# Performance work log

Hardware: AMD Instinct MI355X
Metric: run time of the kernel (lower is better)

The kernel has to match this reference:

```python
import jax, jax.numpy as jnp
import numpy as np

B, LA, LS, C, H = 4, 1536, 512, 256, 4
DK = C // H
NEG = -jnp.inf


def _pad(lengths, maxlen):
    # True where padded (idx >= length)
    return jnp.arange(maxlen)[None, :] >= lengths[:, None]


def build_mask(l_v, l_s, ilens, ylens):
    """Additive float mask [B, l_v+l_s, l_v+l_s] with 0 / -inf, matching
    generate_multi_modal_mask_new."""
    b = ilens.shape[0]
    i = jnp.arange(l_s)
    causal = jnp.where(i[:, None] >= i[None, :], 0.0, NEG)            # [l_s, l_s]
    tgt_pad = _pad(ylens, l_s)                                        # [b, l_s]
    mask_s_s = jnp.where(tgt_pad[:, None, :], NEG, causal[None])      # [b, l_s, l_s]
    src_row = jnp.where(_pad(ilens, l_v), NEG, 0.0)                   # [b, l_v]
    mask_v_v = jnp.broadcast_to(src_row[:, None, :], (b, l_v, l_v))
    mask_s_v = jnp.broadcast_to(src_row[:, None, :], (b, l_s, l_v))
    mask_v_s = jnp.full((b, l_v, l_s), NEG, dtype=jnp.float32)
    top = jnp.concatenate([mask_v_v, mask_v_s], axis=2)
    bot = jnp.concatenate([mask_s_v, mask_s_s], axis=2)
    return jnp.concatenate([top, bot], axis=1)


def setup_inputs() -> dict:
    key = jax.random.key(0)
    ks = jax.random.split(key, 12)
    scale = 1.0 / np.sqrt(C)
    return {
        "audio_encoder_out": jax.random.normal(ks[0], (B, LA, C), jnp.float32),
        "text_encoder_out": jax.random.normal(ks[1], (B, LS, C), jnp.float32),
        "speech_length": jax.random.randint(ks[2], (B,), 1, LA),
        "text_length": jax.random.randint(ks[3], (B,), 1, LS),
        "Wq": jax.random.normal(ks[4], (C, C), jnp.float32) * scale,
        "bq": jax.random.normal(ks[5], (C,), jnp.float32) * scale,
        "Wk": jax.random.normal(ks[6], (C, C), jnp.float32) * scale,
        "bk": jax.random.normal(ks[7], (C,), jnp.float32) * scale,
        "Wv": jax.random.normal(ks[8], (C, C), jnp.float32) * scale,
        "bv": jax.random.normal(ks[9], (C,), jnp.float32) * scale,
        "Wo": jax.random.normal(ks[10], (C, C), jnp.float32) * scale,
        "bo": jax.random.normal(ks[11], (C,), jnp.float32) * scale,
    }


def reference(audio_encoder_out, text_encoder_out, speech_length, text_length,
              Wq, bq, Wk, bk, Wv, bv, Wo, bo):
    b, l_a, c = audio_encoder_out.shape
    l_s = text_encoder_out.shape[1]
    x = jnp.concatenate([audio_encoder_out, text_encoder_out], axis=1)  # [B, L, C]
    L = l_a + l_s

    def heads(W, bias):
        return (x @ W.T + bias).reshape(b, L, H, DK).transpose(0, 2, 1, 3)  # [B,H,L,DK]

    q, k, v = heads(Wq, bq), heads(Wk, bk), heads(Wv, bv)
    scores = jnp.einsum("bhqd,bhkd->bhqk", q, k) / np.float32(np.sqrt(DK))

    amask = build_mask(l_a, l_s, speech_length, text_length)  # additive [B,L,L]
    # Faithful to torch: mask.eq(0) positions (additive-0) are filled with -inf,
    # then zeroed in attn (the module's inverted masking behavior).
    eq0 = (amask == 0.0)[:, None, :, :]                       # [B,1,L,L]
    scores = jnp.where(eq0, NEG, scores)
    attn = jax.nn.softmax(scores, axis=-1)
    attn = jnp.where(eq0, 0.0, attn)                          # (dropout = identity, eval)
    out = jnp.einsum("bhqk,bhkd->bhqd", attn, v)
    out = out.transpose(0, 2, 1, 3).reshape(b, L, H * DK)
    return out @ Wo.T + bo
```

## Files before the change

kernel.cpp:

```cpp
#include <hip/hip_runtime.h>
#include <hip/hip_bf16.h>
#include <math.h>

#define LA 1536
#define LS 512
#define LT 2048
#define CC 256
#define NH 4
#define DKH 64
#define NB 4
#define NT (LT / 64)
#define NTA (LA / 64)
#define SZ ((size_t)NB * LT * CC)

#define QSCALE 0.1803368801111244f

typedef _Float16 f16;
typedef __attribute__((ext_vector_type(8))) _Float16 f16x8;
typedef __attribute__((ext_vector_type(4))) _Float16 f16x4;
typedef __attribute__((ext_vector_type(4))) float f32x4;

__device__ inline f16x8 cvt8(const float4 a, const float4 b) {
    f16x8 h;
    h[0] = (_Float16)a.x; h[1] = (_Float16)a.y; h[2] = (_Float16)a.z; h[3] = (_Float16)a.w;
    h[4] = (_Float16)b.x; h[5] = (_Float16)b.y; h[6] = (_Float16)b.z; h[7] = (_Float16)b.w;
    return h;
}

#define PROW(j) (((j) & 32) | ((((j) >> 2) & 1) << 4) | ((((j) >> 3) & 3) << 2) | ((j) & 3))

__global__ __launch_bounds__(256) void qkv_mfma(
    const float* __restrict__ audio, const float* __restrict__ text,
    const float* __restrict__ Wq, const float* __restrict__ bq,
    const float* __restrict__ Wk, const float* __restrict__ bk,
    const float* __restrict__ Wv, const float* __restrict__ bv,
    f16* __restrict__ Qh, f16* __restrict__ Kh, f16* __restrict__ Vth)
{
    __shared__ f16 smem[128 * 64 + 64 * 64];
    f16* As = smem;
    f16* Bs = smem + 128 * 64;

    const int tid = threadIdx.x;
    const int w = tid >> 6, l = tid & 63;
    const int g = l >> 4, r = l & 15;

    const int m0 = blockIdx.x * 128;
    const int n0 = blockIdx.y * 64;
    const int mat = n0 >> 8;
    const int ch0 = n0 & 255;

    const float* W    = (mat == 0) ? Wq : (mat == 1) ? Wk : Wv;
    const float* bias = (mat == 0) ? bq : (mat == 1) ? bk : bv;

    const int b  = m0 >> 11;
    const int l0 = m0 & 2047;

    f32x4 acc[2][4] = {};

    for (int k0 = 0; k0 < CC; k0 += 64) {
        #pragma unroll
        for (int m = 0; m < 4; ++m) {
            const int idx = m * 256 + tid;
            const int row = idx >> 3, c = idx & 7;
            const int lrow = l0 + row;
            const float* src = (lrow < LA)
                ? (audio + ((size_t)b * LA + lrow) * CC + k0 + c * 8)
                : (text  + ((size_t)b * LS + (lrow - LA)) * CC + k0 + c * 8);
            const float4 x0 = *(const float4*)src;
            const float4 x1 = *(const float4*)(src + 4);
            *(f16x8*)(As + row * 64 + ((c ^ (row & 7)) << 3)) = cvt8(x0, x1);
        }
        #pragma unroll
        for (int m = 0; m < 2; ++m) {
            const int idx = m * 256 + tid;
            const int row = idx >> 3, c = idx & 7;
            const float* src = W + (size_t)(ch0 + row) * CC + k0 + c * 8;
            const float4 x0 = *(const float4*)src;
            const float4 x1 = *(const float4*)(src + 4);
            *(f16x8*)(Bs + row * 64 + ((c ^ (row & 7)) << 3)) = cvt8(x0, x1);
        }
        __syncthreads();
        #pragma unroll
        for (int kc = 0; kc < 2; ++kc) {
            f16x8 af[2];
            #pragma unroll
            for (int i = 0; i < 2; ++i) {
                const int row = w * 32 + i * 16 + r;
                const int c = kc * 4 + g;
                af[i] = *(const f16x8*)(As + row * 64 + ((c ^ (row & 7)) << 3));
            }
            f16x8 bf[4];
            #pragma unroll
            for (int j = 0; j < 4; ++j) {
                const int row = j * 16 + r;
                const int c = kc * 4 + g;
                bf[j] = *(const f16x8*)(Bs + row * 64 + ((c ^ (row & 7)) << 3));
            }
            #pragma unroll
            for (int i = 0; i < 2; ++i)
                #pragma unroll
                for (int j = 0; j < 4; ++j)
                    acc[i][j] = __builtin_amdgcn_mfma_f32_16x16x32_f16(af[i], bf[j], acc[i][j], 0, 0, 0);
        }
        __syncthreads();
    }

    float bcol[4];
    #pragma unroll
    for (int j = 0; j < 4; ++j) bcol[j] = bias[ch0 + j * 16 + r];

    if (mat <= 1) {
        f16* Out = (mat == 0) ? Qh : Kh;
        const float osc = (mat == 0) ? QSCALE : 1.0f;
        #pragma unroll
        for (int i = 0; i < 2; ++i)
            #pragma unroll
            for (int e = 0; e < 4; ++e) {
                const int m = m0 + w * 32 + i * 16 + g * 4 + e;
                #pragma unroll
                for (int j = 0; j < 4; ++j)
                    Out[(size_t)m * CC + ch0 + j * 16 + r] =
                        (_Float16)((acc[i][j][e] + bcol[j]) * osc);
            }
    } else {
        f16* Ts = smem;
        #pragma unroll
        for (int i = 0; i < 2; ++i)
            #pragma unroll
            for (int e = 0; e < 4; ++e) {
                const int ml = w * 32 + i * 16 + g * 4 + e;
                #pragma unroll
                for (int j = 0; j < 4; ++j)
                    Ts[(j * 16 + r) * 136 + ml] = (_Float16)(acc[i][j][e] + bcol[j]);
            }
        __syncthreads();
        const int b2 = m0 >> 11, l0m = m0 & 2047;
        #pragma unroll
        for (int u = 0; u < 4; ++u) {
            const int idx = u * 256 + tid;
            const int nl = idx >> 4, mc = idx & 15;
            const f16x8 vv = *(const f16x8*)(Ts + nl * 136 + mc * 8);
            const int nglob = ch0 + nl;
            const int hh = nglob >> 6, dd = nglob & 63;
            *(f16x8*)(Vth + ((size_t)((b2 * NH + hh) * DKH + dd)) * LT + l0m + mc * 8) = vv;
        }
    }
}

__global__ __launch_bounds__(512) void attn_f16(
    const f16* __restrict__ Q, const f16* __restrict__ K,
    const f16* __restrict__ Vt,
    const int* __restrict__ slen, const int* __restrict__ tlen,
    f16* __restrict__ AO)
{
    __shared__ __align__(16) f16 KsA[2][2 * 4096];
    __shared__ __align__(16) f16 VtsA[2][2 * 4096];

    const int tid = threadIdx.x;
    const int w = tid >> 6, l = tid & 63;
    const int gid = w >> 2, wg = w & 3;
    const int g = l >> 4, r = l & 15;
    const int tg = tid & 255;

    const int q0 = blockIdx.x * 64;
    const int h  = blockIdx.y;
    const int b  = blockIdx.z;

    const int ilen = slen[b];
    const int kcap = LA + tlen[b];
    const int nskip = ilen >> 6;
    int ntskip = 0;
    if (q0 >= LA) {
        const int skipmax = min(q0 - 63, kcap - 64);
        const int d = skipmax - LA;
        ntskip = (d < 0) ? 0 : ((d >> 6) + 1);
    }
    const int nAudio = NTA - nskip;
    const int nProc  = nAudio + (NT - NTA) - ntskip;
    const int nIter  = (nProc + 1) >> 1;

    const int qrow = q0 + 16 * wg + r;

    f16x8 qf[2];
    #pragma unroll
    for (int ch = 0; ch < 2; ++ch)
        qf[ch] = *(const f16x8*)(Q + ((size_t)(b * LT) + qrow) * CC + h * DKH + ch * 32 + g * 8);

    const int srow0 = tg >> 3, scc = tg & 7;
    const int srow1 = srow0 + 32;
    const int kp0 = PROW(srow0), kp1 = PROW(srow1);
    const int kdst0 = kp0 * 64 + ((scc ^ (kp0 & 7)) << 3);
    const int kdst1 = kp1 * 64 + ((scc ^ (kp1 & 7)) << 3);
    const int vdst0 = srow0 * 64 + ((scc ^ (srow0 & 7)) << 3);
    const int vdst1 = srow1 * 64 + ((scc ^ (srow1 & 7)) << 3);

    #define TILE_OF(p) ((p) < nAudio ? (nskip + (p)) : (NTA + ntskip + ((p) - nAudio)))

    {
        const int k0 = TILE_OF(gid) * 64;
        *(f16x8*)(KsA[gid] + kdst0) =
            *(const f16x8*)(K + ((size_t)(b * LT) + k0 + srow0) * CC + h * DKH + scc * 8);
        *(f16x8*)(KsA[gid] + kdst1) =
            *(const f16x8*)(K + ((size_t)(b * LT) + k0 + srow1) * CC + h * DKH + scc * 8);
        *(f16x8*)(VtsA[gid] + vdst0) =
            *(const f16x8*)(Vt + ((size_t)((b * NH + h) * DKH) + srow0) * LT + k0 + scc * 8);
        *(f16x8*)(VtsA[gid] + vdst1) =
            *(const f16x8*)(Vt + ((size_t)((b * NH + h) * DKH) + srow1) * LT + k0 + scc * 8);
    }
    __syncthreads();

    float m_run = -1e30f, l_run = 0.0f;
    f32x4 o[4] = {};

    int cur = 0;
    for (int i = 0; i < nIter; ++i) {
        const int pcur = 2 * i + gid;
        const bool curV = pcur < nProc;
        const bool nxtV = (pcur + 2) < nProc;

        f16x8 kr0, kr1, vr0, vr1;
        if (nxtV) {
            const int kn = TILE_OF(pcur + 2) * 64;
            kr0 = *(const f16x8*)(K + ((size_t)(b * LT) + kn + srow0) * CC + h * DKH + scc * 8);
            kr1 = *(const f16x8*)(K + ((size_t)(b * LT) + kn + srow1) * CC + h * DKH + scc * 8);
            vr0 = *(const f16x8*)(Vt + ((size_t)((b * NH + h) * DKH) + srow0) * LT + kn + scc * 8);
            vr1 = *(const f16x8*)(Vt + ((size_t)((b * NH + h) * DKH) + srow1) * LT + kn + scc * 8);
        }

        if (curV) {
            const int kt = TILE_OF(pcur);
            const int k0 = kt * 64;
            const f16* Kb = KsA[gid] + cur * 4096;
            const f16* Vb = VtsA[gid] + cur * 4096;

            f32x4 sacc[4] = {};
            #pragma unroll
            for (int s = 0; s < 4; ++s) {
                const int arow = 16 * s + r;
                #pragma unroll
                for (int ch = 0; ch < 2; ++ch) {
                    const f16x8 a = *(const f16x8*)(Kb + arow * 64 + (((ch * 4 + g) ^ (arow & 7)) << 3));
                    sacc[s] = __builtin_amdgcn_mfma_f32_16x16x32_f16(a, qf[ch], sacc[s], 0, 0, 0);
                }
            }

            const int mode = (kt < NTA) ? ((k0 >= ilen) ? 0 : 1)
                                        : ((q0 < LA) ? 0 : 2);
            const int kb = k0 + 8 * g;
            float sv[16];
            if (mode == 0) {
                #pragma unroll
                for (int s = 0; s < 4; ++s)
                    #pragma unroll
                    for (int e = 0; e < 4; ++e) sv[s * 4 + e] = sacc[s][e];
            } else if (mode == 1) {
                #pragma unroll
                for (int s = 0; s < 4; ++s)
                    #pragma unroll
                    for (int e = 0; e < 4; ++e) {
                        const int kk = kb + 32 * (s >> 1) + 4 * (s & 1) + e;
                        sv[s * 4 + e] = (kk >= ilen) ? sacc[s][e] : -INFINITY;
                    }
            } else {
                #pragma unroll
                for (int s = 0; s < 4; ++s)
                    #pragma unroll
                    for (int e = 0; e < 4; ++e) {
                        const int kk = kb + 32 * (s >> 1) + 4 * (s & 1) + e;
                        sv[s * 4 + e] = (kk > qrow || kk >= kcap) ? sacc[s][e] : -INFINITY;
                    }
            }

            float mloc = -1e30f;
            #pragma unroll
            for (int u = 0; u < 16; ++u) mloc = fmaxf(mloc, sv[u]);
            mloc = fmaxf(mloc, __shfl_xor(mloc, 16));
            mloc = fmaxf(mloc, __shfl_xor(mloc, 32));
            const float m_new = fmaxf(m_run, mloc);

            float ssum = 0.0f;
            f16x4 ph[4];
            #pragma unroll
            for (int s = 0; s < 4; ++s)
                #pragma unroll
                for (int e = 0; e < 4; ++e) {
                    const float p = exp2f(sv[s * 4 + e] - m_new);
                    ph[s][e] = (_Float16)p;
                    ssum += p;
                }
            ssum += __shfl_xor(ssum, 16);
            ssum += __shfl_xor(ssum, 32);

            if (__all(m_new == m_run)) {
                l_run += ssum;
            } else {
                const float sc = exp2f(m_run - m_new);
                l_run = l_run * sc + ssum;
                m_run = m_new;
                #pragma unroll
                for (int e = 0; e < 4; ++e) {
                    const float scr = __shfl(sc, 4 * g + e);
                    #pragma unroll
                    for (int dsb = 0; dsb < 4; ++dsb) o[dsb][e] *= scr;
                }
            }

            #pragma unroll
            for (int ch = 0; ch < 2; ++ch) {
                f16x8 a;
                #pragma unroll
                for (int e = 0; e < 4; ++e) { a[e] = ph[2 * ch][e]; a[4 + e] = ph[2 * ch + 1][e]; }
                #pragma unroll
                for (int dsb = 0; dsb < 4; ++dsb) {
                    const int vrow = 16 * dsb + r;
                    const f16x8 bf = *(const f16x8*)(Vb + vrow * 64 + (((ch * 4 + g) ^ (vrow & 7)) << 3));
                    o[dsb] = __builtin_amdgcn_mfma_f32_16x16x32_f16(a, bf, o[dsb], 0, 0, 0);
                }
            }
        }

        if (nxtV) {
            f16* Kn = KsA[gid] + (cur ^ 1) * 4096;
            f16* Vn = VtsA[gid] + (cur ^ 1) * 4096;
            *(f16x8*)(Kn + kdst0) = kr0;
            *(f16x8*)(Kn + kdst1) = kr1;
            *(f16x8*)(Vn + vdst0) = vr0;
            *(f16x8*)(Vn + vdst1) = vr1;
        }
        __syncthreads();
        cur ^= 1;
    }

    float* OcF = (float*)&KsA[0][0];
    float* ML1 = (float*)&VtsA[0][0];
    if (gid == 1) {
        #pragma unroll
        for (int dsb = 0; dsb < 4; ++dsb)
            *(f32x4*)(OcF + ((wg * 4 + dsb) << 8) + (l << 2)) = o[dsb];
        if (g == 0) {
            ML1[(16 * wg + r) * 2 + 0] = m_run;
            ML1[(16 * wg + r) * 2 + 1] = l_run;
        }
    }
    __syncthreads();

    if (gid == 0) {
        #pragma unroll
        for (int e = 0; e < 4; ++e) {
            const int qloc = 16 * wg + 4 * g + e;
            const float m0v = __shfl(m_run, 4 * g + e);
            const float l0v = __shfl(l_run, 4 * g + e);
            const float m1v = ML1[qloc * 2 + 0];
            const float l1v = ML1[qloc * 2 + 1];
            const float mt = fmaxf(m0v, m1v);
            const float c0 = exp2f(m0v - mt);
            const float c1 = exp2f(m1v - mt);
            const float inv = 1.0f / (l0v * c0 + l1v * c1);
            #pragma unroll
            for (int dsb = 0; dsb < 4; ++dsb) {
                const float v = (o[dsb][e] * c0
                               + OcF[((wg * 4 + dsb) << 8) + (l << 2) + e] * c1) * inv;
                AO[((size_t)(b * LT) + q0 + qloc) * CC + h * DKH + 16 * dsb + r] = (_Float16)v;
            }
        }
    }
    #undef TILE_OF
}

__global__ __launch_bounds__(256) void out_mfma(
    const f16* __restrict__ X, const float* __restrict__ Wo,
    const float* __restrict__ bo, float* __restrict__ Out)
{
    __shared__ f16 As[128 * 64];
    __shared__ f16 Bs[64 * 64];

    const int tid = threadIdx.x;
    const int w = tid >> 6, l = tid & 63;
    const int g = l >> 4, r = l & 15;

    const int m0 = blockIdx.x * 128;
    const int n0 = blockIdx.y * 64;

    f32x4 acc[2][4] = {};

    for (int k0 = 0; k0 < CC; k0 += 64) {
        #pragma unroll
        for (int m = 0; m < 4; ++m) {
            const int idx = m * 256 + tid;
            const int row = idx >> 3, c = idx & 7;
            *(f16x8*)(As + row * 64 + ((c ^ (row & 7)) << 3)) =
                *(const f16x8*)(X + (size_t)(m0 + row) * CC + k0 + c * 8);
        }
        #pragma unroll
        for (int m = 0; m < 2; ++m) {
            const int idx = m * 256 + tid;
            const int row = idx >> 3, c = idx & 7;
            const float* src = Wo + (size_t)(n0 + row) * CC + k0 + c * 8;
            const float4 x0 = *(const float4*)src;
            const float4 x1 = *(const float4*)(src + 4);
            *(f16x8*)(Bs + row * 64 + ((c ^ (row & 7)) << 3)) = cvt8(x0, x1);
        }
        __syncthreads();
        #pragma unroll
        for (int kc = 0; kc < 2; ++kc) {
            f16x8 af[2];
            #pragma unroll
            for (int i = 0; i < 2; ++i) {
                const int row = w * 32 + i * 16 + r;
                const int c = kc * 4 + g;
                af[i] = *(const f16x8*)(As + row * 64 + ((c ^ (row & 7)) << 3));
            }
            f16x8 bf[4];
            #pragma unroll
            for (int j = 0; j < 4; ++j) {
                const int row = j * 16 + r;
                const int c = kc * 4 + g;
                bf[j] = *(const f16x8*)(Bs + row * 64 + ((c ^ (row & 7)) << 3));
            }
            #pragma unroll
            for (int i = 0; i < 2; ++i)
                #pragma unroll
                for (int j = 0; j < 4; ++j)
                    acc[i][j] = __builtin_amdgcn_mfma_f32_16x16x32_f16(af[i], bf[j], acc[i][j], 0, 0, 0);
        }
        __syncthreads();
    }

    float bcol[4];
    #pragma unroll
    for (int j = 0; j < 4; ++j) bcol[j] = bo[n0 + j * 16 + r];

    #pragma unroll
    for (int i = 0; i < 2; ++i)
        #pragma unroll
        for (int e = 0; e < 4; ++e) {
            const int m = m0 + w * 32 + i * 16 + g * 4 + e;
            #pragma unroll
            for (int j = 0; j < 4; ++j)
                Out[(size_t)m * CC + n0 + j * 16 + r] = acc[i][j][e] + bcol[j];
        }
}

extern "C" void kernel_launch(void* const* d_in, const int* in_sizes, int n_in,
                              void* d_out, int out_size, void* d_ws, size_t ws_size,
                              hipStream_t stream)
{
    const float* audio = (const float*)d_in[0];
    const float* text  = (const float*)d_in[1];
    const int*   slen  = (const int*)d_in[2];
    const int*   tlen  = (const int*)d_in[3];
    const float* Wq = (const float*)d_in[4];
    const float* bq = (const float*)d_in[5];
    const float* Wk = (const float*)d_in[6];
    const float* bk = (const float*)d_in[7];
    const float* Wv = (const float*)d_in[8];
    const float* bv = (const float*)d_in[9];
    const float* Wo = (const float*)d_in[10];
    const float* bo = (const float*)d_in[11];
    float* out = (float*)d_out;

    f16* Qh  = (f16*)d_ws;
    f16* Kh  = Qh + SZ;
    f16* Vth = Kh + SZ;
    f16* AOh = Vth + SZ;

    qkv_mfma<<<dim3(64, 12), 256, 0, stream>>>(audio, text, Wq, bq, Wk, bk, Wv, bv,
                                               Qh, Kh, Vth);
    attn_f16<<<dim3(LT / 64, NH, NB), 512, 0, stream>>>(Qh, Kh, Vth, slen, tlen, AOh);
    out_mfma<<<dim3(64, 4), 256, 0, stream>>>(AOh, Wo, bo, out);
}
```

Measured before the change: 51.13 us.

## Fuse QKV projections per block, single-buffer attention K/V with priority hints

```diff
diff --git a/kernel.cpp b/kernel.cpp
--- a/kernel.cpp
+++ b/kernel.cpp
@@ -36,31 +36,28 @@
     const float* __restrict__ Wv, const float* __restrict__ bv,
     f16* __restrict__ Qh, f16* __restrict__ Kh, f16* __restrict__ Vth)
 {
-    __shared__ f16 smem[128 * 64 + 64 * 64];
+    __shared__ f16 smem[4 * 4096];
     f16* As = smem;
-    f16* Bs = smem + 128 * 64;
 
     const int tid = threadIdx.x;
     const int w = tid >> 6, l = tid & 63;
     const int g = l >> 4, r = l & 15;
 
-    const int m0 = blockIdx.x * 128;
-    const int n0 = blockIdx.y * 64;
-    const int mat = n0 >> 8;
-    const int ch0 = n0 & 255;
-
-    const float* W    = (mat == 0) ? Wq : (mat == 1) ? Wk : Wv;
-    const float* bias = (mat == 0) ? bq : (mat == 1) ? bk : bv;
+    const int m0  = blockIdx.x * 64;
+    const int ch0 = blockIdx.y * 64;
+
+    const float* Ws[3]   = {Wq, Wk, Wv};
+    const float* Bias[3] = {bq, bk, bv};
 
     const int b  = m0 >> 11;
     const int l0 = m0 & 2047;
 
-    f32x4 acc[2][4] = {};
+    f32x4 acc[3][4] = {};
 
     for (int k0 = 0; k0 < CC; k0 += 64) {
         #pragma unroll
-        for (int m = 0; m < 4; ++m) {
-            const int idx = m * 256 + tid;
+        for (int u = 0; u < 2; ++u) {
+            const int idx = u * 256 + tid;
             const int row = idx >> 3, c = idx & 7;
             const int lrow = l0 + row;
             const float* src = (lrow < LA)
@@ -71,79 +68,70 @@
             *(f16x8*)(As + row * 64 + ((c ^ (row & 7)) << 3)) = cvt8(x0, x1);
         }
         #pragma unroll
-        for (int m = 0; m < 2; ++m) {
-            const int idx = m * 256 + tid;
-            const int row = idx >> 3, c = idx & 7;
-            const float* src = W + (size_t)(ch0 + row) * CC + k0 + c * 8;
-            const float4 x0 = *(const float4*)src;
-            const float4 x1 = *(const float4*)(src + 4);
-            *(f16x8*)(Bs + row * 64 + ((c ^ (row & 7)) << 3)) = cvt8(x0, x1);
-        }
+        for (int mat = 0; mat < 3; ++mat)
+            #pragma unroll
+            for (int u = 0; u < 2; ++u) {
+                const int idx = u * 256 + tid;
+                const int row = idx >> 3, c = idx & 7;
+                const float* src = Ws[mat] + (size_t)(ch0 + row) * CC + k0 + c * 8;
+                const float4 x0 = *(const float4*)src;
+                const float4 x1 = *(const float4*)(src + 4);
+                *(f16x8*)(smem + (1 + mat) * 4096 + row * 64 + ((c ^ (row & 7)) << 3)) = cvt8(x0, x1);
+            }
         __syncthreads();
         #pragma unroll
         for (int kc = 0; kc < 2; ++kc) {
-            f16x8 af[2];
-            #pragma unroll
-            for (int i = 0; i < 2; ++i) {
-                const int row = w * 32 + i * 16 + r;
-                const int c = kc * 4 + g;
-                af[i] = *(const f16x8*)(As + row * 64 + ((c ^ (row & 7)) << 3));
-            }
-            f16x8 bf[4];
-            #pragma unroll
-            for (int j = 0; j < 4; ++j) {
-                const int row = j * 16 + r;
-                const int c = kc * 4 + g;
-                bf[j] = *(const f16x8*)(Bs + row * 64 + ((c ^ (row & 7)) << 3));
-            }
-            #pragma unroll
-            for (int i = 0; i < 2; ++i)
-                #pragma unroll
-                for (int j = 0; j < 4; ++j)
-                    acc[i][j] = __builtin_amdgcn_mfma_f32_16x16x32_f16(af[i], bf[j], acc[i][j], 0, 0, 0);
-        }
-        __syncthreads();
-    }
-
-    float bcol[4];
-    #pragma unroll
-    for (int j = 0; j < 4; ++j) bcol[j] = bias[ch0 + j * 16 + r];
-
-    if (mat <= 1) {
-        f16* Out = (mat == 0) ? Qh : Kh;
-        const float osc = (mat == 0) ? QSCALE : 1.0f;
-        #pragma unroll
-        for (int i = 0; i < 2; ++i)
-            #pragma unroll
-            for (int e = 0; e < 4; ++e) {
-                const int m = m0 + w * 32 + i * 16 + g * 4 + e;
-                #pragma unroll
-                for (int j = 0; j < 4; ++j)
-                    Out[(size_t)m * CC + ch0 + j * 16 + r] =
-                        (_Float16)((acc[i][j][e] + bcol[j]) * osc);
-            }
-    } else {
-        f16* Ts = smem;
-        #pragma unroll
-        for (int i = 0; i < 2; ++i)
-            #pragma unroll
-            for (int e = 0; e < 4; ++e) {
-                const int ml = w * 32 + i * 16 + g * 4 + e;
-                #pragma unroll
-                for (int j = 0; j < 4; ++j)
-                    Ts[(j * 16 + r) * 136 + ml] = (_Float16)(acc[i][j][e] + bcol[j]);
-            }
-        __syncthreads();
-        const int b2 = m0 >> 11, l0m = m0 & 2047;
-        #pragma unroll
-        for (int u = 0; u < 4; ++u) {
-            const int idx = u * 256 + tid;
-            const int nl = idx >> 4, mc = idx & 15;
-            const f16x8 vv = *(const f16x8*)(Ts + nl * 136 + mc * 8);
-            const int nglob = ch0 + nl;
-            const int hh = nglob >> 6, dd = nglob & 63;
-            *(f16x8*)(Vth + ((size_t)((b2 * NH + hh) * DKH + dd)) * LT + l0m + mc * 8) = vv;
-        }
+            const int c = kc * 4 + g;
+            const int arow = 16 * w + r;
+            const f16x8 af = *(const f16x8*)(As + arow * 64 + ((c ^ (arow & 7)) << 3));
+            #pragma unroll
+            for (int mat = 0; mat < 3; ++mat)
+                #pragma unroll
+                for (int j = 0; j < 4; ++j) {
+                    const int brow = j * 16 + r;
+                    const f16x8 bf = *(const f16x8*)(smem + (1 + mat) * 4096
+                                                     + brow * 64 + ((c ^ (brow & 7)) << 3));
+                    acc[mat][j] = __builtin_amdgcn_mfma_f32_16x16x32_f16(af, bf, acc[mat][j], 0, 0, 0);
+                }
+        }
+        __syncthreads();
+    }
+
+    float bcol[3][4];
+    #pragma unroll
+    for (int mat = 0; mat < 3; ++mat)
+        #pragma unroll
+        for (int j = 0; j < 4; ++j) bcol[mat][j] = Bias[mat][ch0 + j * 16 + r];
+
+    #pragma unroll
+    for (int e = 0; e < 4; ++e) {
+        const int m = m0 + 16 * w + 4 * g + e;
+        #pragma unroll
+        for (int j = 0; j < 4; ++j) {
+            Qh[(size_t)m * CC + ch0 + j * 16 + r] =
+                (_Float16)((acc[0][j][e] + bcol[0][j]) * QSCALE);
+            Kh[(size_t)m * CC + ch0 + j * 16 + r] =
+                (_Float16)(acc[1][j][e] + bcol[1][j]);
+        }
+    }
+
+    f16* Ts = smem;
+    #pragma unroll
+    for (int e = 0; e < 4; ++e) {
+        const int ml = 16 * w + 4 * g + e;
+        #pragma unroll
+        for (int j = 0; j < 4; ++j)
+            Ts[(j * 16 + r) * 72 + ml] = (_Float16)(acc[2][j][e] + bcol[2][j]);
+    }
+    __syncthreads();
+    #pragma unroll
+    for (int u = 0; u < 2; ++u) {
+        const int idx = u * 256 + tid;
+        const int nl = idx >> 3, mc = idx & 7;
+        const f16x8 vv = *(const f16x8*)(Ts + nl * 72 + mc * 8);
+        const int nglob = ch0 + nl;
+        const int hh = nglob >> 6, dd = nglob & 63;
+        *(f16x8*)(Vth + ((size_t)((b * NH + hh) * DKH + dd)) * LT + l0 + mc * 8) = vv;
     }
 }
 
@@ -153,8 +141,8 @@
     const int* __restrict__ slen, const int* __restrict__ tlen,
     f16* __restrict__ AO)
 {
-    __shared__ __align__(16) f16 KsA[2][2 * 4096];
-    __shared__ __align__(16) f16 VtsA[2][2 * 4096];
+    __shared__ __align__(16) f16 Ks[2][4096];
+    __shared__ __align__(16) f16 Vts[2][4096];
 
     const int tid = threadIdx.x;
     const int w = tid >> 6, l = tid & 63;
@@ -198,22 +186,21 @@
 
     {
         const int k0 = TILE_OF(gid) * 64;
-        *(f16x8*)(KsA[gid] + kdst0) =
+        *(f16x8*)(Ks[gid] + kdst0) =
             *(const f16x8*)(K + ((size_t)(b * LT) + k0 + srow0) * CC + h * DKH + scc * 8);
-        *(f16x8*)(KsA[gid] + kdst1) =
+        *(f16x8*)(Ks[gid] + kdst1) =
             *(const f16x8*)(K + ((size_t)(b * LT) + k0 + srow1) * CC + h * DKH + scc * 8);
-        *(f16x8*)(VtsA[gid] + vdst0) =
+        *(f16x8*)(Vts[gid] + vdst0) =
             *(const f16x8*)(Vt + ((size_t)((b * NH + h) * DKH) + srow0) * LT + k0 + scc * 8);
-        *(f16x8*)(VtsA[gid] + vdst1) =
+        *(f16x8*)(Vts[gid] + vdst1) =
             *(const f16x8*)(Vt + ((size_t)((b * NH + h) * DKH) + srow1) * LT + k0 + scc * 8);
     }
-    __syncthreads();
 
     float m_run = -1e30f, l_run = 0.0f;
     f32x4 o[4] = {};
 
-    int cur = 0;
     for (int i = 0; i < nIter; ++i) {
+        __syncthreads();
         const int pcur = 2 * i + gid;
         const bool curV = pcur < nProc;
         const bool nxtV = (pcur + 2) < nProc;
@@ -230,10 +217,11 @@
         if (curV) {
             const int kt = TILE_OF(pcur);
             const int k0 = kt * 64;
-            const f16* Kb = KsA[gid] + cur * 4096;
-            const f16* Vb = VtsA[gid] + cur * 4096;
+            const f16* Kb = Ks[gid];
+            const f16* Vb = Vts[gid];
 
             f32x4 sacc[4] = {};
+            __builtin_amdgcn_s_setprio(1);
             #pragma unroll
             for (int s = 0; s < 4; ++s) {
                 const int arow = 16 * s + r;
@@ -243,6 +231,7 @@
                     sacc[s] = __builtin_amdgcn_mfma_f32_16x16x32_f16(a, qf[ch], sacc[s], 0, 0, 0);
                 }
             }
+            __builtin_amdgcn_s_setprio(0);
 
             const int mode = (kt < NTA) ? ((k0 >= ilen) ? 0 : 1)
                                         : ((q0 < LA) ? 0 : 2);
@@ -305,6 +294,7 @@
                 }
             }
 
+            __builtin_amdgcn_s_setprio(1);
             #pragma unroll
             for (int ch = 0; ch < 2; ++ch) {
                 f16x8 a;
@@ -317,22 +307,20 @@
                     o[dsb] = __builtin_amdgcn_mfma_f32_16x16x32_f16(a, bf, o[dsb], 0, 0, 0);
                 }
             }
-        }
-
+            __builtin_amdgcn_s_setprio(0);
+        }
+
+        __syncthreads();
         if (nxtV) {
-            f16* Kn = KsA[gid] + (cur ^ 1) * 4096;
-            f16* Vn = VtsA[gid] + (cur ^ 1) * 4096;
-            *(f16x8*)(Kn + kdst0) = kr0;
-            *(f16x8*)(Kn + kdst1) = kr1;
-            *(f16x8*)(Vn + vdst0) = vr0;
-            *(f16x8*)(Vn + vdst1) = vr1;
-        }
-        __syncthreads();
-        cur ^= 1;
-    }
-
-    float* OcF = (float*)&KsA[0][0];
-    float* ML1 = (float*)&VtsA[0][0];
+            *(f16x8*)(Ks[gid] + kdst0)  = kr0;
+            *(f16x8*)(Ks[gid] + kdst1)  = kr1;
+            *(f16x8*)(Vts[gid] + vdst0) = vr0;
+            *(f16x8*)(Vts[gid] + vdst1) = vr1;
+        }
+    }
+
+    float* OcF = (float*)&Ks[0][0];
+    float* ML1 = (float*)&Vts[0][0];
     if (gid == 1) {
         #pragma unroll
         for (int dsb = 0; dsb < 4; ++dsb)
@@ -464,7 +452,7 @@
     f16* Vth = Kh + SZ;
     f16* AOh = Vth + SZ;
 
-    qkv_mfma<<<dim3(64, 12), 256, 0, stream>>>(audio, text, Wq, bq, Wk, bk, Wv, bv,
+    qkv_mfma<<<dim3(128, 4), 256, 0, stream>>>(audio, text, Wq, bq, Wk, bk, Wv, bv,
                                                Qh, Kh, Vth);
     attn_f16<<<dim3(LT / 64, NH, NB), 512, 0, stream>>>(Qh, Kh, Vth, slen, tlen, AOh);
     out_mfma<<<dim3(64, 4), 256, 0, stream>>>(AOh, Wo, bo, out);
```

Result: slower. 54.67 us (+6.9%).
